# Performance work log

Measured on AMD Instinct MI355X. Metric: run time of the kernel, lower is better.

## Reference

```python
import jax, jax.numpy as jnp
import numpy as np
from jax import lax

SEQ_LEN, BATCH, Z_DIM, X_DIM = 512, 256, 64, 10000


def setup_inputs() -> dict:
    key = jax.random.key(0)
    k1, k2, k3, k4 = jax.random.split(key, 4)
    inp = jax.random.randint(k1, (SEQ_LEN, BATCH), 0, X_DIM)
    # Row-stochastic transition matrix so probability mass is conserved by alpha @ T.T
    T = jax.random.uniform(k2, (Z_DIM, Z_DIM), dtype=jnp.float32)
    T = T / T.sum(axis=1, keepdims=True)
    pi = jax.random.uniform(k3, (Z_DIM,), dtype=jnp.float32)
    pi = pi / pi.sum()
    # Emission weights near 1.0 so the unnormalized recursion stays in fp32 range
    emit = 0.7 + 0.6 * jax.random.uniform(k4, (X_DIM, Z_DIM), dtype=jnp.float32)
    return {"input": inp, "T": T, "pi": pi, "emit": emit}


def reference(input, T, pi, emit):
    # input: [S, B] int; emit: [X, Z]; T: [Z, Z]; pi: [Z]
    e = emit[input]                      # [S, B, Z] gather of emission weights
    alpha0 = e[0] * pi[None, :]          # [B, Z]

    def fwd_step(a_prev, e_t):
        a_t = e_t * (a_prev @ T.T)       # [B, Z]
        return a_t, a_t

    _, alphas = lax.scan(fwd_step, alpha0, e[1:])
    alpha = jnp.concatenate([alpha0[None], alphas], axis=0)  # [S, B, Z]

    beta_last = jnp.ones_like(alpha0)    # beta[S-1] = 1

    def bwd_step(b_next, e_t1):
        b_t = (e_t1 * b_next) @ T        # [B, Z]
        return b_t, b_t

    # xs[t] = e[t+1]; reverse scan yields beta[t] for t = 0..S-2 in order
    _, betas = lax.scan(bwd_step, beta_last, e[1:], reverse=True)
    beta = jnp.concatenate([betas, beta_last[None]], axis=0)  # [S, B, Z]

    ab = alpha * beta
    posterior_marginal = ab / ab.sum(-1, keepdims=True)
    return alpha, beta, posterior_marginal
```

## Files before the change

### kernel.cpp

```cpp
#include <hip/hip_runtime.h>
#include <hip/hip_bf16.h>

#define SEQ   512
#define BATCH 256
#define ZD    64

typedef float vfloat4 __attribute__((ext_vector_type(4)));

__device__ __forceinline__ float lane_bcastf(float v, int i) {
  return __int_as_float(__builtin_amdgcn_readlane(__float_as_int(v), i));
}
__device__ __forceinline__ int lane_bcasti(int v, int i) {
  return __builtin_amdgcn_readlane(v, i);
}

#define REP8(M,p)  M(p##0) M(p##1) M(p##2) M(p##3) M(p##4) M(p##5) M(p##6) M(p##7)
#define REP64(M)   REP8(M,0) REP8(M,1) REP8(M,2) REP8(M,3) \
                   REP8(M,4) REP8(M,5) REP8(M,6) REP8(M,7)

#define TDECL(n)  float t##n;
#define TLOADF(n) t##n = Trp[0##n];
#define TLOADB(n) t##n = Tcp[(0##n) * ZD];
#define TFMA(n)   acc[(0##n) & 3] = fmaf(lane_bcastf(vbc, 0##n), t##n, acc[(0##n) & 3]);
#define TPIN(p)   asm volatile("" : "+v"(t##p##0), "+v"(t##p##1), "+v"(t##p##2), \
                                    "+v"(t##p##3), "+v"(t##p##4), "+v"(t##p##5), \
                                    "+v"(t##p##6), "+v"(t##p##7));
#define TPIN_ALL  TPIN(0) TPIN(1) TPIN(2) TPIN(3) TPIN(4) TPIN(5) TPIN(6) TPIN(7)

__global__ __launch_bounds__(64, 1) void hmm_chains(
    const int*   __restrict__ inp,
    const float* __restrict__ T,
    const float* __restrict__ pi,
    const float* __restrict__ emit,
    float* __restrict__ out_alpha,
    float* __restrict__ out_beta)
{
  const int lane = threadIdx.x;
  const int blk  = blockIdx.x;
  const bool fwd = (blk < BATCH);
  const int b    = fwd ? blk : blk - BATCH;

  REP64(TDECL)

  if (fwd) {
    int xvn[8];
    #pragma unroll
    for (int w = 0; w < 8; ++w) {
      int li = w * 64 + lane + 1;
      if (li > SEQ - 1) li = SEQ - 1;
      xvn[w] = inp[li * BATCH + b];
    }

    const float* Trp = T + lane * ZD;
    REP64(TLOADF)
    TPIN_ALL

    const int x0 = inp[b];
    float alpha = emit[x0 * ZD + lane] * pi[lane];
    float* op = out_alpha + (size_t)b * ZD + lane;

    const int x1 = lane_bcasti(xvn[0], 0);
    float e_cur = emit[x1 * ZD + lane];
    __builtin_nontemporal_store(alpha, op);
    op += BATCH * ZD;

    #pragma unroll
    for (int w = 0; w < 8; ++w) {
      const int xnw = xvn[w];
      #pragma unroll 1
      for (int idx = (w == 0) ? 1 : 0; idx < 64; ++idx) {
        const int   xt1  = lane_bcasti(xnw, idx);
        const float e_pf = emit[xt1 * ZD + lane];
        float acc[4] = {0.f, 0.f, 0.f, 0.f};
        const float vbc = alpha;
        REP64(TFMA)
        alpha = e_cur * ((acc[0] + acc[1]) + (acc[2] + acc[3]));
        __builtin_nontemporal_store(alpha, op);
        op += BATCH * ZD;
        e_cur = e_pf;
      }
    }
  } else {
    int xv[8];
    #pragma unroll
    for (int w = 0; w < 8; ++w)
      xv[w] = inp[(w * 64 + lane) * BATCH + b];

    const float* Tcp = T + lane;
    REP64(TLOADB)
    TPIN_ALL

    float beta = 1.0f;
    float* op = out_beta + ((size_t)(SEQ - 1) * BATCH + b) * ZD + lane;
    __builtin_nontemporal_store(beta, op);
    op -= BATCH * ZD;

    const int xL = lane_bcasti(xv[7], 63);
    float e_next = emit[xL * ZD + lane];

    #pragma unroll
    for (int w = 7; w >= 0; --w) {
      const int xvw = xv[w];
      #pragma unroll 1
      for (int idx = (w == 7) ? 62 : 63; idx >= 0; --idx) {
        const int   xt   = lane_bcasti(xvw, idx);
        const float e_pf = emit[xt * ZD + lane];
        const float vbc  = e_next * beta;
        float acc[4] = {0.f, 0.f, 0.f, 0.f};
        REP64(TFMA)
        beta = (acc[0] + acc[1]) + (acc[2] + acc[3]);
        __builtin_nontemporal_store(beta, op);
        op -= BATCH * ZD;
        e_next = e_pf;
      }
    }
  }
}

__global__ __launch_bounds__(256) void posterior_k(
    const float* __restrict__ a,
    const float* __restrict__ bt,
    float*       __restrict__ p)
{
  const int tid = blockIdx.x * 256 + threadIdx.x;
  const size_t base = (size_t)tid * 8;

  const vfloat4 va0 = __builtin_nontemporal_load(reinterpret_cast<const vfloat4*>(a  + base));
  const vfloat4 va1 = __builtin_nontemporal_load(reinterpret_cast<const vfloat4*>(a  + base + 4));
  const vfloat4 vb0 = __builtin_nontemporal_load(reinterpret_cast<const vfloat4*>(bt + base));
  const vfloat4 vb1 = __builtin_nontemporal_load(reinterpret_cast<const vfloat4*>(bt + base + 4));

  const float p0 = va0.x * vb0.x;
  const float p1 = va0.y * vb0.y;
  const float p2 = va0.z * vb0.z;
  const float p3 = va0.w * vb0.w;
  const float p4 = va1.x * vb1.x;
  const float p5 = va1.y * vb1.y;
  const float p6 = va1.z * vb1.z;
  const float p7 = va1.w * vb1.w;

  float s = ((p0 + p1) + (p2 + p3)) + ((p4 + p5) + (p6 + p7));
  s += __shfl_xor(s, 1);
  s += __shfl_xor(s, 2);
  s += __shfl_xor(s, 4);
  const float inv = 1.0f / s;

  vfloat4 o0, o1;
  o0.x = p0 * inv; o0.y = p1 * inv; o0.z = p2 * inv; o0.w = p3 * inv;
  o1.x = p4 * inv; o1.y = p5 * inv; o1.z = p6 * inv; o1.w = p7 * inv;
  __builtin_nontemporal_store(o0, reinterpret_cast<vfloat4*>(p + base));
  __builtin_nontemporal_store(o1, reinterpret_cast<vfloat4*>(p + base + 4));
}

extern "C" void kernel_launch(void* const* d_in, const int* in_sizes, int n_in,
                              void* d_out, int out_size, void* d_ws, size_t ws_size,
                              hipStream_t stream) {
  const int*   inp  = (const int*)  d_in[0];
  const float* T    = (const float*)d_in[1];
  const float* pi   = (const float*)d_in[2];
  const float* emit = (const float*)d_in[3];

  float* out = (float*)d_out;
  const size_t N = (size_t)SEQ * BATCH * ZD;
  float* out_alpha = out;
  float* out_beta  = out + N;
  float* out_post  = out + 2 * N;

  hipLaunchKernelGGL(hmm_chains, dim3(2 * BATCH), dim3(64), 0, stream,
                     inp, T, pi, emit, out_alpha, out_beta);

  hipLaunchKernelGGL(posterior_k, dim3((unsigned)(N / 2048)), dim3(256), 0, stream,
                     out_alpha, out_beta, out_post);
}
```

Before: 250.1 us.

## Broadcast state via LDS and use packed FMA instead of readlane chain

```diff
diff --git a/kernel.cpp b/kernel.cpp
--- a/kernel.cpp
+++ b/kernel.cpp
@@ -5,27 +5,31 @@
 #define BATCH 256
 #define ZD    64
 
+typedef float vfloat2 __attribute__((ext_vector_type(2)));
 typedef float vfloat4 __attribute__((ext_vector_type(4)));
 
-__device__ __forceinline__ float lane_bcastf(float v, int i) {
-  return __int_as_float(__builtin_amdgcn_readlane(__float_as_int(v), i));
-}
 __device__ __forceinline__ int lane_bcasti(int v, int i) {
   return __builtin_amdgcn_readlane(v, i);
 }
 
 #define REP8(M,p)  M(p##0) M(p##1) M(p##2) M(p##3) M(p##4) M(p##5) M(p##6) M(p##7)
-#define REP64(M)   REP8(M,0) REP8(M,1) REP8(M,2) REP8(M,3) \
-                   REP8(M,4) REP8(M,5) REP8(M,6) REP8(M,7)
+#define REP16(M)   REP8(M,0) REP8(M,1)
 
-#define TDECL(n)  float t##n;
-#define TLOADF(n) t##n = Trp[0##n];
-#define TLOADB(n) t##n = Tcp[(0##n) * ZD];
-#define TFMA(n)   acc[(0##n) & 3] = fmaf(lane_bcastf(vbc, 0##n), t##n, acc[(0##n) & 3]);
-#define TPIN(p)   asm volatile("" : "+v"(t##p##0), "+v"(t##p##1), "+v"(t##p##2), \
-                                    "+v"(t##p##3), "+v"(t##p##4), "+v"(t##p##5), \
-                                    "+v"(t##p##6), "+v"(t##p##7));
-#define TPIN_ALL  TPIN(0) TPIN(1) TPIN(2) TPIN(3) TPIN(4) TPIN(5) TPIN(6) TPIN(7)
+#define UDECL(n)  vfloat2 ua##n, ub##n;
+#define ULOADF(n) ua##n = *(const vfloat2*)(Trp + 4*(0##n)); \
+                  ub##n = *(const vfloat2*)(Trp + 4*(0##n) + 2);
+#define ULOADB(n) ua##n = (vfloat2){Tcp[(4*(0##n)+0)*ZD], Tcp[(4*(0##n)+1)*ZD]}; \
+                  ub##n = (vfloat2){Tcp[(4*(0##n)+2)*ZD], Tcp[(4*(0##n)+3)*ZD]};
+#define UFMA(n)   { const vfloat4 rb = *(const vfloat4*)(albuf + 4*(0##n)); \
+                    acc01 = __builtin_elementwise_fma((vfloat2){rb.x, rb.y}, ua##n, acc01); \
+                    acc23 = __builtin_elementwise_fma((vfloat2){rb.z, rb.w}, ub##n, acc23); }
+#define UPIN(p)   asm volatile("" : "+v"(ua##p##0), "+v"(ua##p##1), "+v"(ua##p##2), \
+                                    "+v"(ua##p##3), "+v"(ua##p##4), "+v"(ua##p##5), \
+                                    "+v"(ua##p##6), "+v"(ua##p##7), \
+                                    "+v"(ub##p##0), "+v"(ub##p##1), "+v"(ub##p##2), \
+                                    "+v"(ub##p##3), "+v"(ub##p##4), "+v"(ub##p##5), \
+                                    "+v"(ub##p##6), "+v"(ub##p##7));
+#define UPIN_ALL  UPIN(0) UPIN(1)
 
 __global__ __launch_bounds__(64, 1) void hmm_chains(
     const int*   __restrict__ inp,
@@ -40,7 +44,9 @@
   const bool fwd = (blk < BATCH);
   const int b    = fwd ? blk : blk - BATCH;
 
-  REP64(TDECL)
+  __shared__ alignas(16) float albuf[ZD];
+
+  REP16(UDECL)
 
   if (fwd) {
     int xvn[8];
@@ -52,8 +58,8 @@
     }
 
     const float* Trp = T + lane * ZD;
-    REP64(TLOADF)
-    TPIN_ALL
+    REP16(ULOADF)
+    UPIN_ALL
 
     const int x0 = inp[b];
     float alpha = emit[x0 * ZD + lane] * pi[lane];
@@ -71,10 +77,10 @@
       for (int idx = (w == 0) ? 1 : 0; idx < 64; ++idx) {
         const int   xt1  = lane_bcasti(xnw, idx);
         const float e_pf = emit[xt1 * ZD + lane];
-        float acc[4] = {0.f, 0.f, 0.f, 0.f};
-        const float vbc = alpha;
-        REP64(TFMA)
-        alpha = e_cur * ((acc[0] + acc[1]) + (acc[2] + acc[3]));
+        albuf[lane] = alpha;
+        vfloat2 acc01 = {0.f, 0.f}, acc23 = {0.f, 0.f};
+        REP16(UFMA)
+        alpha = e_cur * ((acc01.x + acc01.y) + (acc23.x + acc23.y));
         __builtin_nontemporal_store(alpha, op);
         op += BATCH * ZD;
         e_cur = e_pf;
@@ -87,8 +93,8 @@
       xv[w] = inp[(w * 64 + lane) * BATCH + b];
 
     const float* Tcp = T + lane;
-    REP64(TLOADB)
-    TPIN_ALL
+    REP16(ULOADB)
+    UPIN_ALL
 
     float beta = 1.0f;
     float* op = out_beta + ((size_t)(SEQ - 1) * BATCH + b) * ZD + lane;
@@ -105,10 +111,11 @@
       for (int idx = (w == 7) ? 62 : 63; idx >= 0; --idx) {
         const int   xt   = lane_bcasti(xvw, idx);
         const float e_pf = emit[xt * ZD + lane];
-        const float vbc  = e_next * beta;
-        float acc[4] = {0.f, 0.f, 0.f, 0.f};
-        REP64(TFMA)
-        beta = (acc[0] + acc[1]) + (acc[2] + acc[3]);
+        const float g    = e_next * beta;
+        albuf[lane] = g;
+        vfloat2 acc01 = {0.f, 0.f}, acc23 = {0.f, 0.f};
+        REP16(UFMA)
+        beta = (acc01.x + acc01.y) + (acc23.x + acc23.y);
         __builtin_nontemporal_store(beta, op);
         op -= BATCH * ZD;
         e_next = e_pf;
```

Measured after the change: 312.6 us. +25.0%, slower.
